# Optimization experiments

Hardware: AMD Instinct MI355X
Metric: run time of the kernel (lower is better)

Reference implementation:

```python
import jax, jax.numpy as jnp
import numpy as np

N_HEAD = 16
N_KV = 4
HEAD_DIM = 128
N_EMBD = 2048
GATE_CH = 32


def setup_inputs() -> dict:
    key = jax.random.key(0)
    ks = jax.random.split(key, 9)
    B, T = 2, 2048
    return {
        "x": jax.random.normal(ks[0], (B, T, N_EMBD), jnp.float32),
        "ve": jax.random.normal(ks[1], (B, T, N_KV * HEAD_DIM), jnp.float32),
        "cos": jax.random.uniform(ks[2], (T, 1, HEAD_DIM // 2), jnp.float32),
        "sin": jax.random.uniform(ks[3], (T, 1, HEAD_DIM // 2), jnp.float32),
        "wq": jax.random.normal(ks[4], (N_HEAD * HEAD_DIM, N_EMBD), jnp.float32) * 0.02,
        "wk": jax.random.normal(ks[5], (N_KV * HEAD_DIM, N_EMBD), jnp.float32) * 0.02,
        "wv": jax.random.normal(ks[6], (N_KV * HEAD_DIM, N_EMBD), jnp.float32) * 0.02,
        "wo": jax.random.normal(ks[7], (N_EMBD, N_EMBD), jnp.float32) * 0.02,
        "wgate": jax.random.normal(ks[8], (N_KV, GATE_CH), jnp.float32) * 0.02,
        "window_size": 512,
    }


def _rope(t, cos, sin):
    half = t.shape[-1] // 2
    t1, t2 = t[..., :half], t[..., half:]
    return jnp.concatenate([t1 * cos + t2 * sin, -t1 * sin + t2 * cos], axis=-1)


def _rms(t):
    eps = jnp.finfo(t.dtype).eps
    return t * jax.lax.rsqrt(jnp.mean(t * t, axis=-1, keepdims=True) + eps)


def reference(x, ve, cos, sin, wq, wk, wv, wo, wgate, window_size):
    B, T, _ = x.shape
    q = (x @ wq.T).reshape(B, T, N_HEAD, HEAD_DIM)
    k = (x @ wk.T).reshape(B, T, N_KV, HEAD_DIM)
    v = (x @ wv.T).reshape(B, T, N_KV, HEAD_DIM)
    # value-embedding gate
    gate = 2.0 * jax.nn.sigmoid(x[..., :GATE_CH] @ wgate.T)  # [B,T,N_KV]
    v = v + gate[..., None] * ve.reshape(B, T, N_KV, HEAD_DIM)
    # RoPE then QK RMSNorm
    q = _rms(_rope(q, cos, sin)).transpose(0, 2, 1, 3)  # [B,H,T,D]
    k = _rms(_rope(k, cos, sin)).transpose(0, 2, 1, 3)  # [B,KV,T,D]
    v = v.transpose(0, 2, 1, 3)
    rep = N_HEAD // N_KV
    k = jnp.repeat(k, rep, axis=1)  # repeat_interleave over head dim
    v = jnp.repeat(v, rep, axis=1)
    # sliding-window causal mask (past_len=0, key_len=T)
    pos = jnp.arange(T)
    mask = (pos[None, :] <= pos[:, None]) & (pos[None, :] >= pos[:, None] - window_size + 1)
    scale = 1.0 / jnp.sqrt(jnp.float32(HEAD_DIM))
    scores = jnp.einsum("bhqd,bhkd->bhqk", q, k) * scale
    scores = jnp.where(mask[None, None], scores, jnp.finfo(scores.dtype).min)
    attn = jax.nn.softmax(scores, axis=-1)
    y = jnp.einsum("bhqk,bhkd->bhqd", attn, v)
    y = y.transpose(0, 2, 1, 3).reshape(B, T, N_EMBD)
    return y @ wo.T
```

## Files before the change

### kernel.cpp

```cpp
#include <hip/hip_runtime.h>
#include <hip/hip_bf16.h>

typedef __attribute__((ext_vector_type(8))) short short8_t;
typedef __attribute__((ext_vector_type(4))) float f32x4;
typedef __attribute__((ext_vector_type(16))) float f32x16;
using bf16 = __hip_bfloat16;

#define MFMA_BF16(A, B, C) __builtin_amdgcn_mfma_f32_16x16x32_bf16((A), (B), (C), 0, 0, 0)
#define MFMA32_BF16(A, B, C) __builtin_amdgcn_mfma_f32_32x32x16_bf16((A), (B), (C), 0, 0, 0)

#define GLD_LDS16(g, l)                                                        \
  __builtin_amdgcn_global_load_lds(                                           \
      (const __attribute__((address_space(1))) unsigned int*)(const void*)(g),\
      (__attribute__((address_space(3))) unsigned int*)(void*)(l), 16, 0, 0)

__device__ __forceinline__ float bits2f(short s) {
  union { unsigned int u; float f; } c;
  c.u = ((unsigned int)(unsigned short)s) << 16;
  return c.f;
}
__device__ __forceinline__ short f2bits(float f) {
  bf16 h = __float2bfloat16(f);
  return *reinterpret_cast<short*>(&h);
}
__device__ __forceinline__ unsigned pack2(float lo, float hi) {
  return ((unsigned)(unsigned short)f2bits(lo)) |
         (((unsigned)(unsigned short)f2bits(hi)) << 16);
}
__device__ __forceinline__ float exp2_(float x) {
#if __has_builtin(__builtin_amdgcn_exp2f)
  return __builtin_amdgcn_exp2f(x);
#else
  return exp2f(x);
#endif
}

__global__ __launch_bounds__(256) void cvt_f32_bf16(const float* __restrict__ in,
                                                    short* __restrict__ out, int n) {
  int i = (blockIdx.x * 256 + threadIdx.x) * 4;
  if (i >= n) return;
  float4 v = *reinterpret_cast<const float4*>(in + i);
  short4 o;
  o.x = f2bits(v.x); o.y = f2bits(v.y); o.z = f2bits(v.z); o.w = f2bits(v.w);
  *reinterpret_cast<short4*>(out + i) = o;
}

__global__ __launch_bounds__(256) void cvt_w3(const float* __restrict__ wq,
                                              const float* __restrict__ wk,
                                              const float* __restrict__ wv,
                                              short* __restrict__ out) {
  int i = (blockIdx.x * 256 + threadIdx.x) * 4;
  const float* src;
  int off;
  if (i < 4194304) { src = wq; off = i; }
  else if (i < 5242880) { src = wk; off = i - 4194304; }
  else { src = wv; off = i - 5242880; }
  float4 v = *reinterpret_cast<const float4*>(src + off);
  short4 o;
  o.x = f2bits(v.x); o.y = f2bits(v.y); o.z = f2bits(v.z); o.w = f2bits(v.w);
  *reinterpret_cast<short4*>(out + i) = o;
}

template <int STORE_BF16>
__global__ __launch_bounds__(128, 2) void gemm_bt5(const short* __restrict__ A,
                                                   const short* __restrict__ Bt,
                                                   void* __restrict__ C,
                                                   int M, int N, int K, int NBN) {
  __shared__ __align__(16) short lds[3 * 8192];
  const int nwg = gridDim.x;
  const int cpx = nwg >> 3;
  const int wg = ((int)blockIdx.x & 7) * cpx + ((int)blockIdx.x >> 3);
  const int m0 = (wg / NBN) * 128, n0 = (wg % NBN) * 128;

  const int tid = threadIdx.x, w = tid >> 6, lane = tid & 63;
  const int rr = lane & 15, g = lane >> 4;

  const int srow = tid >> 2;
  const int sg = (tid & 3) ^ (srow & 3);
  const short* Asrc = A + (size_t)(m0 + srow) * K + sg * 8;
  const short* Bsrc = Bt + (size_t)(n0 + srow) * K + sg * 8;
  const int dofs = tid * 16;

  const int xorg = ((g ^ (rr & 3)) << 4);
  const int abase = rr * 64 + xorg;
  const int bbase = 8192 + w * 4096 + rr * 64 + xorg;

  f32x4 acc[8][4];
#pragma unroll
  for (int mi = 0; mi < 8; ++mi)
#pragma unroll
    for (int ni = 0; ni < 4; ++ni) acc[mi][ni] = (f32x4){0.f, 0.f, 0.f, 0.f};

  const int ns = K >> 5;

#define STG5(s_, base_) do {                                                   \
    const short* a_ = Asrc + (size_t)(s_) * 32;                                \
    const short* b_ = Bsrc + (size_t)(s_) * 32;                                \
    char* d_ = (char*)lds + (base_) + dofs;                                    \
    GLD_LDS16(a_,                  d_);                                        \
    GLD_LDS16(a_ + (size_t)32 * K, d_ + 2048);                                 \
    GLD_LDS16(a_ + (size_t)64 * K, d_ + 4096);                                 \
    GLD_LDS16(a_ + (size_t)96 * K, d_ + 6144);                                 \
    GLD_LDS16(b_,                  d_ + 8192);                                 \
    GLD_LDS16(b_ + (size_t)32 * K, d_ + 10240);                                \
    GLD_LDS16(b_ + (size_t)64 * K, d_ + 12288);                                \
    GLD_LDS16(b_ + (size_t)96 * K, d_ + 14336);                                \
  } while (0)

  STG5(0, 0);
  if (ns > 1) STG5(1, 16384);
  asm volatile("s_waitcnt vmcnt(8)" ::: "memory");
  asm volatile("s_barrier" ::: "memory");

  int c0 = 0, c1 = 16384, c2 = 32768;
  for (int s = 0; s < ns; ++s) {
    const char* bufp = (const char*)lds + c0;
    short8_t a0 = *(const short8_t*)(bufp + abase);
    short8_t a1 = *(const short8_t*)(bufp + abase + 1024);
    short8_t a2 = *(const short8_t*)(bufp + abase + 2048);
    short8_t a3 = *(const short8_t*)(bufp + abase + 3072);
    short8_t a4 = *(const short8_t*)(bufp + abase + 4096);
    short8_t a5 = *(const short8_t*)(bufp + abase + 5120);
    short8_t a6 = *(const short8_t*)(bufp + abase + 6144);
    short8_t a7 = *(const short8_t*)(bufp + abase + 7168);
    short8_t b0 = *(const short8_t*)(bufp + bbase);
    short8_t b1 = *(const short8_t*)(bufp + bbase + 1024);
    short8_t b2 = *(const short8_t*)(bufp + bbase + 2048);
    short8_t b3 = *(const short8_t*)(bufp + bbase + 3072);

    if (s + 2 < ns) STG5(s + 2, c2);

    asm volatile("s_waitcnt lgkmcnt(0)" ::: "memory");
    __builtin_amdgcn_sched_barrier(0);
    __builtin_amdgcn_s_setprio(1);
    acc[0][0] = MFMA_BF16(a0, b0, acc[0][0]);
    acc[0][1] = MFMA_BF16(a0, b1, acc[0][1]);
    acc[0][2] = MFMA_BF16(a0, b2, acc[0][2]);
    acc[0][3] = MFMA_BF16(a0, b3, acc[0][3]);
    acc[1][0] = MFMA_BF16(a1, b0, acc[1][0]);
    acc[1][1] = MFMA_BF16(a1, b1, acc[1][1]);
    acc[1][2] = MFMA_BF16(a1, b2, acc[1][2]);
    acc[1][3] = MFMA_BF16(a1, b3, acc[1][3]);
    acc[2][0] = MFMA_BF16(a2, b0, acc[2][0]);
    acc[2][1] = MFMA_BF16(a2, b1, acc[2][1]);
    acc[2][2] = MFMA_BF16(a2, b2, acc[2][2]);
    acc[2][3] = MFMA_BF16(a2, b3, acc[2][3]);
    acc[3][0] = MFMA_BF16(a3, b0, acc[3][0]);
    acc[3][1] = MFMA_BF16(a3, b1, acc[3][1]);
    acc[3][2] = MFMA_BF16(a3, b2, acc[3][2]);
    acc[3][3] = MFMA_BF16(a3, b3, acc[3][3]);
    acc[4][0] = MFMA_BF16(a4, b0, acc[4][0]);
    acc[4][1] = MFMA_BF16(a4, b1, acc[4][1]);
    acc[4][2] = MFMA_BF16(a4, b2, acc[4][2]);
    acc[4][3] = MFMA_BF16(a4, b3, acc[4][3]);
    acc[5][0] = MFMA_BF16(a5, b0, acc[5][0]);
    acc[5][1] = MFMA_BF16(a5, b1, acc[5][1]);
    acc[5][2] = MFMA_BF16(a5, b2, acc[5][2]);
    acc[5][3] = MFMA_BF16(a5, b3, acc[5][3]);
    acc[6][0] = MFMA_BF16(a6, b0, acc[6][0]);
    acc[6][1] = MFMA_BF16(a6, b1, acc[6][1]);
    acc[6][2] = MFMA_BF16(a6, b2, acc[6][2]);
    acc[6][3] = MFMA_BF16(a6, b3, acc[6][3]);
    acc[7][0] = MFMA_BF16(a7, b0, acc[7][0]);
    acc[7][1] = MFMA_BF16(a7, b1, acc[7][1]);
    acc[7][2] = MFMA_BF16(a7, b2, acc[7][2]);
    acc[7][3] = MFMA_BF16(a7, b3, acc[7][3]);
    __builtin_amdgcn_s_setprio(0);

    if (s + 2 < ns)
      asm volatile("s_waitcnt vmcnt(8)" ::: "memory");
    else if (s + 1 < ns)
      asm volatile("s_waitcnt vmcnt(0)" ::: "memory");
    asm volatile("s_barrier" ::: "memory");
    int t_ = c0; c0 = c1; c1 = c2; c2 = t_;
  }
#undef STG5

#pragma unroll
  for (int mi = 0; mi < 8; ++mi)
#pragma unroll
    for (int ni = 0; ni < 4; ++ni) {
      const int row = m0 + mi * 16 + g * 4;
      const int col = n0 + w * 64 + ni * 16 + rr;
#pragma unroll
      for (int j = 0; j < 4; ++j) {
        float v = acc[mi][ni][j];
        if (STORE_BF16)
          reinterpret_cast<short*>(C)[(size_t)(row + j) * N + col] = f2bits(v);
        else
          reinterpret_cast<float*>(C)[(size_t)(row + j) * N + col] = v;
      }
    }
}

__global__ __launch_bounds__(256) void rope_rms_qk(const short* __restrict__ qkv,
                                                   const float* __restrict__ cosT,
                                                   const float* __restrict__ sinT,
                                                   short* __restrict__ qO,
                                                   short* __restrict__ kO) {
  const int T = 2048;
  int unit = blockIdx.x * 4 + (threadIdx.x >> 6);
  int lane = threadIdx.x & 63;
  int hh = unit % 20;
  int t = (unit / 20) % T;
  int b = unit / (20 * T);
  int col = hh < 16 ? hh * 128 : 2048 + (hh - 16) * 128;
  const short* src = qkv + (size_t)(b * T + t) * 3072 + col;
  float t1 = bits2f(src[lane]), t2 = bits2f(src[lane + 64]);
  float c = cosT[t * 64 + lane], s = sinT[t * 64 + lane];
  float o1 = t1 * c + t2 * s;
  float o2 = t2 * c - t1 * s;
  float ss = o1 * o1 + o2 * o2;
#pragma unroll
  for (int o = 1; o < 64; o <<= 1) ss += __shfl_xor(ss, o, 64);
  float r = rsqrtf(ss * (1.f / 128.f) + 1.1920929e-07f);
  short* dst;
  if (hh < 16) {
    r *= 0.08838834764831845f * 1.4426950408889634f;
    dst = qO + ((size_t)(b * 16 + hh) * T + t) * 128;
  } else {
    dst = kO + ((size_t)(b * 4 + (hh - 16)) * T + t) * 128;
  }
  dst[lane] = f2bits(o1 * r);
  dst[lane + 64] = f2bits(o2 * r);
}

__global__ __launch_bounds__(256) void v_gate(const short* __restrict__ qkv,
                                              const float* __restrict__ x,
                                              const float* __restrict__ ve,
                                              const float* __restrict__ wgate,
                                              short* __restrict__ vO) {
  const int T = 2048;
  int unit = blockIdx.x * 4 + (threadIdx.x >> 6);
  int lane = threadIdx.x & 63;
  int kv = unit & 3;
  int t = (unit >> 2) % T;
  int b = unit / (4 * T);
  size_t m = (size_t)b * T + t;
  float z = 0.f;
  if (lane < 32) z = x[m * 2048 + lane] * wgate[kv * 32 + lane];
#pragma unroll
  for (int o = 1; o < 64; o <<= 1) z += __shfl_xor(z, o, 64);
  float gate = 2.f / (1.f + __expf(-z));
  const short* vsrc = qkv + m * 3072 + 2560 + kv * 128;
  const float* vesrc = ve + m * 512 + kv * 128;
  short* dst = vO + ((size_t)(b * 4 + kv) * T + t) * 128;
  dst[lane] = f2bits(bits2f(vsrc[lane]) + gate * vesrc[lane]);
  dst[lane + 64] = f2bits(bits2f(vsrc[lane + 64]) + gate * vesrc[lane + 64]);
}

__global__ __launch_bounds__(256) void v_transpose(const short* __restrict__ vp,
                                                   short* __restrict__ vT) {
  const int T = 2048;
  int bkv = blockIdx.x & 7;
  int t0 = (blockIdx.x >> 3) * 64;
  __shared__ __align__(16) short L[128 * 64];
  int tid = threadIdx.x;
  int tt = tid >> 2, dblk = tid & 3;
  const short* src = vp + ((size_t)bkv * T + t0 + tt) * 128 + dblk * 32;
  short8_t v0 = *(const short8_t*)(src);
  short8_t v1 = *(const short8_t*)(src + 8);
  short8_t v2 = *(const short8_t*)(src + 16);
  short8_t v3 = *(const short8_t*)(src + 24);
#pragma unroll
  for (int i = 0; i < 32; ++i) {
    int d = dblk * 32 + i;
    int byte = (d * 128 + tt * 2) ^ ((d & 7) << 4);
    short val = i < 8 ? v0[i] : i < 16 ? v1[i - 8] : i < 24 ? v2[i - 16] : v3[i - 24];
    *(short*)((char*)L + byte) = val;
  }
  __syncthreads();
  int d = tid >> 1, th = tid & 1;
  const char* Lp = (const char*)L;
#pragma unroll
  for (int g2 = 0; g2 < 4; ++g2) {
    short8_t o = *(const short8_t*)(Lp + ((d * 128 + th * 64 + g2 * 16) ^ ((d & 7) << 4)));
    *(short8_t*)(vT + ((size_t)bkv * 128 + d) * T + t0 + th * 32 + g2 * 8) = o;
  }
}

__global__ __launch_bounds__(256) void attn_sw3(const short* __restrict__ Q,
                                                const short* __restrict__ K,
                                                const short* __restrict__ VT,
                                                short* __restrict__ Y,
                                                const int* __restrict__ winp) {
  const int T = 2048, H = 16;
  const int win = *winp;
  int combo = blockIdx.x & 7;
  int j = blockIdx.x >> 3;
  int b = combo >> 2, kvh = combo & 3;
  int h = kvh * 4 + (j & 3);
  int q0 = (15 - (j >> 2)) * 128;

  __shared__ __align__(16) short Ks[2][64 * 128];
  __shared__ __align__(16) short Vs[2][128 * 64];

  int tid = threadIdx.x, w = tid >> 6, lane = tid & 63;
  int ql = lane & 31, hi = lane >> 5;
  int qrow = q0 + w * 32 + ql;

  const short* qbase = Q + ((size_t)(b * H + h) * T + qrow) * 128;
  short8_t qf[8];
#pragma unroll
  for (int ks = 0; ks < 8; ++ks)
    qf[ks] = *reinterpret_cast<const short8_t*>(qbase + ks * 16 + hi * 8);

  const short* kbase = K + (size_t)(b * 4 + kvh) * T * 128;
  const short* vtbase = VT + (size_t)(b * 4 + kvh) * 128 * T;

  f32x16 acc[4];
#pragma unroll
  for (int dt = 0; dt < 4; ++dt)
#pragma unroll
    for (int r = 0; r < 16; ++r) acc[dt][r] = 0.f;
  float mreg = -1e30f, lsum = 0.f;

  int lo = q0 - win + 1;
  if (lo < 0) lo = 0;
  lo &= ~63;
  const int nt = (q0 + 128 - lo) >> 6;
  int qmin = q0 + w * 32, qmax = qmin + 31;

#define STAGE_A(ti, bi) do {                                                   \
    int kc_ = lo + (ti) * 64;                                                  \
    _Pragma("unroll")                                                          \
    for (int r = 0; r < 4; ++r) {                                              \
      int slot = (r * 4 + w) * 64 + lane;                                      \
      int krow = slot >> 4;                                                    \
      int gc = (slot & 15) ^ (krow & 7);                                       \
      GLD_LDS16(kbase + (size_t)(kc_ + krow) * 128 + gc * 8,                   \
                (char*)Ks[bi] + (r * 4 + w) * 1024);                           \
    }                                                                          \
    _Pragma("unroll")                                                          \
    for (int r = 0; r < 4; ++r) {                                              \
      int slot = (r * 4 + w) * 64 + lane;                                      \
      int d_ = slot >> 3;                                                      \
      int gc = (slot & 7) ^ (d_ & 7);                                          \
      GLD_LDS16(vtbase + (size_t)d_ * T + kc_ + gc * 8,                        \
                (char*)Vs[bi] + (r * 4 + w) * 1024);                           \
    }                                                                          \
  } while (0)

  STAGE_A(0, 0);

  int cur = 0;
  for (int t = 0; t < nt; ++t) {
    if (t + 1 < nt) {
      STAGE_A(t + 1, cur ^ 1);
      asm volatile("s_waitcnt vmcnt(8)" ::: "memory");
    } else {
      asm volatile("s_waitcnt vmcnt(0)" ::: "memory");
    }
    asm volatile("s_barrier" ::: "memory");

    int kc = lo + t * 64;
    bool active = (kc <= qmax) && (kc + 63 >= qmin - win + 1);
    if (active) {
      const char* Kp = (const char*)Ks[cur];
      const char* Vp = (const char*)Vs[cur];
      f32x16 sA[2];
#pragma unroll
      for (int r = 0; r < 16; ++r) { sA[0][r] = 0.f; sA[1][r] = 0.f; }
#pragma unroll
      for (int kt = 0; kt < 2; ++kt) {
        int kr = kt * 32 + ql;
#pragma unroll
        for (int ks = 0; ks < 8; ++ks) {
          int byte = kr * 256 + (((ks * 2 + hi) ^ (kr & 7)) << 4);
          short8_t kf = *reinterpret_cast<const short8_t*>(Kp + byte);
          sA[kt] = MFMA32_BF16(kf, qf[ks], sA[kt]);
        }
      }
      float pmax = -1e30f;
#pragma unroll
      for (int kt = 0; kt < 2; ++kt)
#pragma unroll
        for (int r = 0; r < 16; ++r) {
          int key = kc + kt * 32 + (r & 3) + 8 * (r >> 2) + 4 * hi;
          float sv = sA[kt][r];
          sv = ((unsigned)(qrow - key) < (unsigned)win) ? sv : -1e30f;
          sA[kt][r] = sv;
          pmax = fmaxf(pmax, sv);
        }
      pmax = fmaxf(pmax, __shfl_xor(pmax, 32, 64));
      float mn = fmaxf(mreg, pmax);
      float corr = exp2_(mreg - mn);
      mreg = mn;
      float rs = 0.f;
#pragma unroll
      for (int kt = 0; kt < 2; ++kt)
#pragma unroll
        for (int r = 0; r < 16; ++r) {
          float p = exp2_(sA[kt][r] - mn);
          sA[kt][r] = p;
          rs += p;
        }
      rs += __shfl_xor(rs, 32, 64);
      lsum = lsum * corr + rs;
#pragma unroll
      for (int dt = 0; dt < 4; ++dt)
#pragma unroll
        for (int r = 0; r < 16; ++r) acc[dt][r] *= corr;

#pragma unroll
      for (int kt = 0; kt < 2; ++kt)
#pragma unroll
        for (int s = 0; s < 2; ++s) {
          unsigned a = pack2(sA[kt][8 * s + 0], sA[kt][8 * s + 1]);
          unsigned bb = pack2(sA[kt][8 * s + 2], sA[kt][8 * s + 3]);
          unsigned c = pack2(sA[kt][8 * s + 4], sA[kt][8 * s + 5]);
          unsigned dd = pack2(sA[kt][8 * s + 6], sA[kt][8 * s + 7]);
          unsigned sa = __shfl_xor(a, 32, 64);
          unsigned sb = __shfl_xor(bb, 32, 64);
          unsigned sc2 = __shfl_xor(c, 32, 64);
          unsigned sd = __shfl_xor(dd, 32, 64);
          union { unsigned u[4]; short8_t s8; } pu;
          pu.u[0] = hi ? sc2 : a;
          pu.u[1] = hi ? sd : bb;
          pu.u[2] = hi ? c : sa;
          pu.u[3] = hi ? dd : sb;
          const int kst = kt * 2 + s;
#pragma unroll
          for (int dt = 0; dt < 4; ++dt) {
            int d_ = dt * 32 + ql;
            int byte = (d_ << 7) + ((((kst * 2 + hi)) ^ (d_ & 7)) << 4);
            short8_t vf = *reinterpret_cast<const short8_t*>(Vp + byte);
            acc[dt] = MFMA32_BF16(vf, pu.s8, acc[dt]);
          }
        }
    }
    asm volatile("s_barrier" ::: "memory");
    cur ^= 1;
  }
#undef STAGE_A

  float rinv = 1.f / lsum;
  short* ybase = Y + ((size_t)(b * T + qrow) * H + h) * 128;
#pragma unroll
  for (int dt = 0; dt < 4; ++dt)
#pragma unroll
    for (int g2 = 0; g2 < 4; ++g2) {
      short4 o;
      o.x = f2bits(acc[dt][g2 * 4 + 0] * rinv);
      o.y = f2bits(acc[dt][g2 * 4 + 1] * rinv);
      o.z = f2bits(acc[dt][g2 * 4 + 2] * rinv);
      o.w = f2bits(acc[dt][g2 * 4 + 3] * rinv);
      *reinterpret_cast<short4*>(ybase + dt * 32 + 8 * g2 + 4 * hi) = o;
    }
}

extern "C" void kernel_launch(void* const* d_in, const int* in_sizes, int n_in,
                              void* d_out, int out_size, void* d_ws, size_t ws_size,
                              hipStream_t stream) {
  const float* x = (const float*)d_in[0];
  const float* ve = (const float*)d_in[1];
  const float* cosT = (const float*)d_in[2];
  const float* sinT = (const float*)d_in[3];
  const float* wq = (const float*)d_in[4];
  const float* wk = (const float*)d_in[5];
  const float* wv = (const float*)d_in[6];
  const float* wo = (const float*)d_in[7];
  const float* wgate = (const float*)d_in[8];
  const int* winp = (const int*)d_in[9];
  float* out = (float*)d_out;
  char* ws = (char*)d_ws;

  const int B = 2, T = 2048;
  short* xb    = (short*)(ws);
  short* wqkvb = (short*)(ws + 16777216);
  short* wob   = (short*)(ws + 29360128);
  short* qkv   = (short*)(ws + 37748736);
  short* qpost = (short*)(ws + 62914560);
  short* kpost = (short*)(ws + 79691776);
  short* vpost = (short*)(ws + 83886080);
  short* ybuf  = (short*)(ws + 88080384);
  short* vTb   = qkv;

  cvt_f32_bf16<<<dim3(8192), 256, 0, stream>>>(x, xb, B * T * 2048);
  cvt_w3<<<dim3(6144), 256, 0, stream>>>(wq, wk, wv, wqkvb);
  cvt_f32_bf16<<<dim3(4096), 256, 0, stream>>>(wo, wob, 2048 * 2048);

  gemm_bt5<1><<<dim3(768), 128, 0, stream>>>(xb, wqkvb, qkv, 4096, 3072, 2048, 24);

  rope_rms_qk<<<dim3(B * T * 20 / 4), 256, 0, stream>>>(qkv, cosT, sinT, qpost, kpost);
  v_gate<<<dim3(B * T), 256, 0, stream>>>(qkv, x, ve, wgate, vpost);
  v_transpose<<<dim3(8 * (T / 64)), 256, 0, stream>>>(vpost, vTb);

  attn_sw3<<<dim3(512), 256, 0, stream>>>(qpost, kpost, vTb, ybuf, winp);

  gemm_bt5<0><<<dim3(512), 128, 0, stream>>>(ybuf, wob, out, 4096, 2048, 2048, 16);
}
```

Before: 197.3 us.

## Enlarge GEMM tile to 256x128 with 4 waves and fuse V gate with transpose

The GEMM now uses 256-thread workgroups computing 256x128 tiles, with a 2x2 wave layout. The three-stage LDS ring is restructured so the next stage's global-to-LDS loads are issued in two halves interleaved with two MFMA phases, and there is a single barrier per iteration. Separately, the value-embedding gate and the V transpose are fused into one kernel, which removes an intermediate buffer round-trip and a launch. Larger tiles halve the grid (384 and 256 blocks), which risks worse CU occupancy and tail balance on a 256-CU part.

```diff
diff --git a/kernel.cpp b/kernel.cpp
--- a/kernel.cpp
+++ b/kernel.cpp
@@ -62,28 +62,29 @@
 }
 
 template <int STORE_BF16>
-__global__ __launch_bounds__(128, 2) void gemm_bt5(const short* __restrict__ A,
+__global__ __launch_bounds__(256, 2) void gemm_bt6(const short* __restrict__ A,
                                                    const short* __restrict__ Bt,
                                                    void* __restrict__ C,
                                                    int M, int N, int K, int NBN) {
-  __shared__ __align__(16) short lds[3 * 8192];
+  __shared__ __align__(16) short lds[3 * 12288];
   const int nwg = gridDim.x;
   const int cpx = nwg >> 3;
   const int wg = ((int)blockIdx.x & 7) * cpx + ((int)blockIdx.x >> 3);
-  const int m0 = (wg / NBN) * 128, n0 = (wg % NBN) * 128;
+  const int m0 = (wg / NBN) * 256, n0 = (wg % NBN) * 128;
 
   const int tid = threadIdx.x, w = tid >> 6, lane = tid & 63;
+  const int wm = w >> 1, wn = w & 1;
   const int rr = lane & 15, g = lane >> 4;
 
-  const int srow = tid >> 2;
-  const int sg = (tid & 3) ^ (srow & 3);
-  const short* Asrc = A + (size_t)(m0 + srow) * K + sg * 8;
-  const short* Bsrc = Bt + (size_t)(n0 + srow) * K + sg * 8;
+  const int srow4 = tid >> 2;
+  const int scol = ((tid & 3) ^ (srow4 & 3)) * 8;
+  const short* Asrc = A + (size_t)(m0 + srow4) * K + scol;
+  const short* Bsrc = Bt + (size_t)(n0 + srow4) * K + scol;
+  const size_t rstep = (size_t)64 * K;
   const int dofs = tid * 16;
 
-  const int xorg = ((g ^ (rr & 3)) << 4);
-  const int abase = rr * 64 + xorg;
-  const int bbase = 8192 + w * 4096 + rr * 64 + xorg;
+  const int abase = ((((wm * 128 + rr) << 6) | (g << 4)) ^ ((rr & 3) << 4));
+  const int bbase = 16384 + ((((wn * 64 + rr) << 6) | (g << 4)) ^ ((rr & 3) << 4));
 
   f32x4 acc[8][4];
 #pragma unroll
@@ -93,95 +94,110 @@
 
   const int ns = K >> 5;
 
-#define STG5(s_, base_) do {                                                   \
+#define STG_FULL(s_, base_) do {                                               \
     const short* a_ = Asrc + (size_t)(s_) * 32;                                \
     const short* b_ = Bsrc + (size_t)(s_) * 32;                                \
     char* d_ = (char*)lds + (base_) + dofs;                                    \
-    GLD_LDS16(a_,                  d_);                                        \
-    GLD_LDS16(a_ + (size_t)32 * K, d_ + 2048);                                 \
-    GLD_LDS16(a_ + (size_t)64 * K, d_ + 4096);                                 \
-    GLD_LDS16(a_ + (size_t)96 * K, d_ + 6144);                                 \
-    GLD_LDS16(b_,                  d_ + 8192);                                 \
-    GLD_LDS16(b_ + (size_t)32 * K, d_ + 10240);                                \
-    GLD_LDS16(b_ + (size_t)64 * K, d_ + 12288);                                \
-    GLD_LDS16(b_ + (size_t)96 * K, d_ + 14336);                                \
+    GLD_LDS16(a_,             d_);                                             \
+    GLD_LDS16(a_ + rstep,     d_ + 4096);                                      \
+    GLD_LDS16(a_ + 2 * rstep, d_ + 8192);                                      \
+    GLD_LDS16(a_ + 3 * rstep, d_ + 12288);                                     \
+    GLD_LDS16(b_,             d_ + 16384);                                     \
+    GLD_LDS16(b_ + rstep,     d_ + 20480);                                     \
   } while (0)
 
-  STG5(0, 0);
-  if (ns > 1) STG5(1, 16384);
-  asm volatile("s_waitcnt vmcnt(8)" ::: "memory");
-  asm volatile("s_barrier" ::: "memory");
-
-  int c0 = 0, c1 = 16384, c2 = 32768;
+  STG_FULL(0, 0);
+  if (ns > 1) STG_FULL(1, 24576);
+  asm volatile("s_waitcnt vmcnt(6)" ::: "memory");
+
+  int sl = 0;
   for (int s = 0; s < ns; ++s) {
-    const char* bufp = (const char*)lds + c0;
-    short8_t a0 = *(const short8_t*)(bufp + abase);
-    short8_t a1 = *(const short8_t*)(bufp + abase + 1024);
-    short8_t a2 = *(const short8_t*)(bufp + abase + 2048);
-    short8_t a3 = *(const short8_t*)(bufp + abase + 3072);
-    short8_t a4 = *(const short8_t*)(bufp + abase + 4096);
-    short8_t a5 = *(const short8_t*)(bufp + abase + 5120);
-    short8_t a6 = *(const short8_t*)(bufp + abase + 6144);
-    short8_t a7 = *(const short8_t*)(bufp + abase + 7168);
-    short8_t b0 = *(const short8_t*)(bufp + bbase);
-    short8_t b1 = *(const short8_t*)(bufp + bbase + 1024);
-    short8_t b2 = *(const short8_t*)(bufp + bbase + 2048);
-    short8_t b3 = *(const short8_t*)(bufp + bbase + 3072);
-
-    if (s + 2 < ns) STG5(s + 2, c2);
-
+    asm volatile("s_barrier" ::: "memory");
+    const char* Ap = (const char*)lds + sl;
+    int sl2 = sl + 49152; if (sl2 >= 73728) sl2 -= 73728;
+    const bool more = (s + 2) < ns;
+    const short* a2 = Asrc + (size_t)(s + 2) * 32;
+    const short* b2 = Bsrc + (size_t)(s + 2) * 32;
+    char* d2 = (char*)lds + sl2 + dofs;
+
+    short8_t b0 = *(const short8_t*)(Ap + bbase);
+    short8_t b1 = *(const short8_t*)(Ap + bbase + 1024);
+    short8_t b2f = *(const short8_t*)(Ap + bbase + 2048);
+    short8_t b3 = *(const short8_t*)(Ap + bbase + 3072);
+    short8_t a0 = *(const short8_t*)(Ap + abase);
+    short8_t a1 = *(const short8_t*)(Ap + abase + 1024);
+    short8_t a2f = *(const short8_t*)(Ap + abase + 2048);
+    short8_t a3 = *(const short8_t*)(Ap + abase + 3072);
+    if (more) {
+      GLD_LDS16(a2, d2);
+      GLD_LDS16(a2 + rstep, d2 + 4096);
+    }
     asm volatile("s_waitcnt lgkmcnt(0)" ::: "memory");
     __builtin_amdgcn_sched_barrier(0);
     __builtin_amdgcn_s_setprio(1);
     acc[0][0] = MFMA_BF16(a0, b0, acc[0][0]);
     acc[0][1] = MFMA_BF16(a0, b1, acc[0][1]);
-    acc[0][2] = MFMA_BF16(a0, b2, acc[0][2]);
+    acc[0][2] = MFMA_BF16(a0, b2f, acc[0][2]);
     acc[0][3] = MFMA_BF16(a0, b3, acc[0][3]);
     acc[1][0] = MFMA_BF16(a1, b0, acc[1][0]);
     acc[1][1] = MFMA_BF16(a1, b1, acc[1][1]);
-    acc[1][2] = MFMA_BF16(a1, b2, acc[1][2]);
+    acc[1][2] = MFMA_BF16(a1, b2f, acc[1][2]);
     acc[1][3] = MFMA_BF16(a1, b3, acc[1][3]);
-    acc[2][0] = MFMA_BF16(a2, b0, acc[2][0]);
-    acc[2][1] = MFMA_BF16(a2, b1, acc[2][1]);
-    acc[2][2] = MFMA_BF16(a2, b2, acc[2][2]);
-    acc[2][3] = MFMA_BF16(a2, b3, acc[2][3]);
+    acc[2][0] = MFMA_BF16(a2f, b0, acc[2][0]);
+    acc[2][1] = MFMA_BF16(a2f, b1, acc[2][1]);
+    acc[2][2] = MFMA_BF16(a2f, b2f, acc[2][2]);
+    acc[2][3] = MFMA_BF16(a2f, b3, acc[2][3]);
     acc[3][0] = MFMA_BF16(a3, b0, acc[3][0]);
     acc[3][1] = MFMA_BF16(a3, b1, acc[3][1]);
-    acc[3][2] = MFMA_BF16(a3, b2, acc[3][2]);
+    acc[3][2] = MFMA_BF16(a3, b2f, acc[3][2]);
     acc[3][3] = MFMA_BF16(a3, b3, acc[3][3]);
+    __builtin_amdgcn_s_setprio(0);
+
+    short8_t a4 = *(const short8_t*)(Ap + abase + 4096);
+    short8_t a5 = *(const short8_t*)(Ap + abase + 5120);
+    short8_t a6 = *(const short8_t*)(Ap + abase + 6144);
+    short8_t a7 = *(const short8_t*)(Ap + abase + 7168);
+    if (more) {
+      GLD_LDS16(a2 + 2 * rstep, d2 + 8192);
+      GLD_LDS16(a2 + 3 * rstep, d2 + 12288);
+      GLD_LDS16(b2, d2 + 16384);
+      GLD_LDS16(b2 + rstep, d2 + 20480);
+    }
+    asm volatile("s_waitcnt lgkmcnt(0)" ::: "memory");
+    __builtin_amdgcn_sched_barrier(0);
+    __builtin_amdgcn_s_setprio(1);
     acc[4][0] = MFMA_BF16(a4, b0, acc[4][0]);
     acc[4][1] = MFMA_BF16(a4, b1, acc[4][1]);
-    acc[4][2] = MFMA_BF16(a4, b2, acc[4][2]);
+    acc[4][2] = MFMA_BF16(a4, b2f, acc[4][2]);
     acc[4][3] = MFMA_BF16(a4, b3, acc[4][3]);
     acc[5][0] = MFMA_BF16(a5, b0, acc[5][0]);
     acc[5][1] = MFMA_BF16(a5, b1, acc[5][1]);
-    acc[5][2] = MFMA_BF16(a5, b2, acc[5][2]);
+    acc[5][2] = MFMA_BF16(a5, b2f, acc[5][2]);
     acc[5][3] = MFMA_BF16(a5, b3, acc[5][3]);
     acc[6][0] = MFMA_BF16(a6, b0, acc[6][0]);
     acc[6][1] = MFMA_BF16(a6, b1, acc[6][1]);
-    acc[6][2] = MFMA_BF16(a6, b2, acc[6][2]);
+    acc[6][2] = MFMA_BF16(a6, b2f, acc[6][2]);
     acc[6][3] = MFMA_BF16(a6, b3, acc[6][3]);
     acc[7][0] = MFMA_BF16(a7, b0, acc[7][0]);
     acc[7][1] = MFMA_BF16(a7, b1, acc[7][1]);
-    acc[7][2] = MFMA_BF16(a7, b2, acc[7][2]);
+    acc[7][2] = MFMA_BF16(a7, b2f, acc[7][2]);
     acc[7][3] = MFMA_BF16(a7, b3, acc[7][3]);
     __builtin_amdgcn_s_setprio(0);
 
-    if (s + 2 < ns)
-      asm volatile("s_waitcnt vmcnt(8)" ::: "memory");
+    if (more)
+      asm volatile("s_waitcnt vmcnt(6)" ::: "memory");
     else if (s + 1 < ns)
       asm volatile("s_waitcnt vmcnt(0)" ::: "memory");
-    asm volatile("s_barrier" ::: "memory");
-    int t_ = c0; c0 = c1; c1 = c2; c2 = t_;
+    sl += 24576; if (sl >= 73728) sl -= 73728;
   }
-#undef STG5
+#undef STG_FULL
 
 #pragma unroll
   for (int mi = 0; mi < 8; ++mi)
 #pragma unroll
     for (int ni = 0; ni < 4; ++ni) {
-      const int row = m0 + mi * 16 + g * 4;
-      const int col = n0 + w * 64 + ni * 16 + rr;
+      const int row = m0 + wm * 128 + mi * 16 + g * 4;
+      const int col = n0 + wn * 64 + ni * 16 + rr;
 #pragma unroll
       for (int j = 0; j < 4; ++j) {
         float v = acc[mi][ni][j];
@@ -225,49 +241,43 @@
   dst[lane + 64] = f2bits(o2 * r);
 }
 
-__global__ __launch_bounds__(256) void v_gate(const short* __restrict__ qkv,
-                                              const float* __restrict__ x,
-                                              const float* __restrict__ ve,
-                                              const float* __restrict__ wgate,
-                                              short* __restrict__ vO) {
-  const int T = 2048;
-  int unit = blockIdx.x * 4 + (threadIdx.x >> 6);
-  int lane = threadIdx.x & 63;
-  int kv = unit & 3;
-  int t = (unit >> 2) % T;
-  int b = unit / (4 * T);
-  size_t m = (size_t)b * T + t;
-  float z = 0.f;
-  if (lane < 32) z = x[m * 2048 + lane] * wgate[kv * 32 + lane];
-#pragma unroll
-  for (int o = 1; o < 64; o <<= 1) z += __shfl_xor(z, o, 64);
-  float gate = 2.f / (1.f + __expf(-z));
-  const short* vsrc = qkv + m * 3072 + 2560 + kv * 128;
-  const float* vesrc = ve + m * 512 + kv * 128;
-  short* dst = vO + ((size_t)(b * 4 + kv) * T + t) * 128;
-  dst[lane] = f2bits(bits2f(vsrc[lane]) + gate * vesrc[lane]);
-  dst[lane + 64] = f2bits(bits2f(vsrc[lane + 64]) + gate * vesrc[lane + 64]);
-}
-
-__global__ __launch_bounds__(256) void v_transpose(const short* __restrict__ vp,
-                                                   short* __restrict__ vT) {
+__global__ __launch_bounds__(256) void vgate_t(const short* __restrict__ qkv,
+                                               const float* __restrict__ x,
+                                               const float* __restrict__ ve,
+                                               const float* __restrict__ wgate,
+                                               short* __restrict__ vT) {
   const int T = 2048;
   int bkv = blockIdx.x & 7;
   int t0 = (blockIdx.x >> 3) * 64;
+  int b = bkv >> 2, kv = bkv & 3;
   __shared__ __align__(16) short L[128 * 64];
   int tid = threadIdx.x;
-  int tt = tid >> 2, dblk = tid & 3;
-  const short* src = vp + ((size_t)bkv * T + t0 + tt) * 128 + dblk * 32;
-  short8_t v0 = *(const short8_t*)(src);
-  short8_t v1 = *(const short8_t*)(src + 8);
-  short8_t v2 = *(const short8_t*)(src + 16);
-  short8_t v3 = *(const short8_t*)(src + 24);
+  int tt = tid >> 2, q = tid & 3;
+  size_t m = (size_t)b * T + t0 + tt;
+  float z = 0.f;
+  const float* xp = x + m * 2048 + q * 8;
+  const float* wgp = wgate + kv * 32 + q * 8;
+#pragma unroll
+  for (int i = 0; i < 8; ++i) z += xp[i] * wgp[i];
+  z += __shfl_xor(z, 1, 64);
+  z += __shfl_xor(z, 2, 64);
+  float gate = 2.f / (1.f + __expf(-z));
+  const short* vsrc = qkv + m * 3072 + 2560 + kv * 128 + q * 32;
+  const float* vesrc = ve + m * 512 + kv * 128 + q * 32;
+  short8_t v0 = *(const short8_t*)(vsrc);
+  short8_t v1 = *(const short8_t*)(vsrc + 8);
+  short8_t v2 = *(const short8_t*)(vsrc + 16);
+  short8_t v3 = *(const short8_t*)(vsrc + 24);
+  float4 e[8];
+#pragma unroll
+  for (int i = 0; i < 8; ++i) e[i] = *(const float4*)(vesrc + i * 4);
 #pragma unroll
   for (int i = 0; i < 32; ++i) {
-    int d = dblk * 32 + i;
+    int d = q * 32 + i;
+    short vv = i < 8 ? v0[i] : i < 16 ? v1[i - 8] : i < 24 ? v2[i - 16] : v3[i - 24];
+    float ev = (&e[i >> 2].x)[i & 3];
     int byte = (d * 128 + tt * 2) ^ ((d & 7) << 4);
-    short val = i < 8 ? v0[i] : i < 16 ? v1[i - 8] : i < 24 ? v2[i - 16] : v3[i - 24];
-    *(short*)((char*)L + byte) = val;
+    *(short*)((char*)L + byte) = f2bits(bits2f(vv) + gate * ev);
   }
   __syncthreads();
   int d = tid >> 1, th = tid & 1;
@@ -472,21 +482,19 @@
   short* qkv   = (short*)(ws + 37748736);
   short* qpost = (short*)(ws + 62914560);
   short* kpost = (short*)(ws + 79691776);
-  short* vpost = (short*)(ws + 83886080);
+  short* vTb   = (short*)(ws + 83886080);
   short* ybuf  = (short*)(ws + 88080384);
-  short* vTb   = qkv;
 
   cvt_f32_bf16<<<dim3(8192), 256, 0, stream>>>(x, xb, B * T * 2048);
   cvt_w3<<<dim3(6144), 256, 0, stream>>>(wq, wk, wv, wqkvb);
   cvt_f32_bf16<<<dim3(4096), 256, 0, stream>>>(wo, wob, 2048 * 2048);
 
-  gemm_bt5<1><<<dim3(768), 128, 0, stream>>>(xb, wqkvb, qkv, 4096, 3072, 2048, 24);
+  gemm_bt6<1><<<dim3(384), 256, 0, stream>>>(xb, wqkvb, qkv, 4096, 3072, 2048, 24);
 
   rope_rms_qk<<<dim3(B * T * 20 / 4), 256, 0, stream>>>(qkv, cosT, sinT, qpost, kpost);
-  v_gate<<<dim3(B * T), 256, 0, stream>>>(qkv, x, ve, wgate, vpost);
-  v_transpose<<<dim3(8 * (T / 64)), 256, 0, stream>>>(vpost, vTb);
+  vgate_t<<<dim3(8 * (T / 64)), 256, 0, stream>>>(qkv, x, ve, wgate, vTb);
 
   attn_sw3<<<dim3(512), 256, 0, stream>>>(qpost, kpost, vTb, ybuf, winp);
 
-  gemm_bt5<0><<<dim3(512), 128, 0, stream>>>(ybuf, wob, out, 4096, 2048, 2048, 16);
-}
+  gemm_bt6<0><<<dim3(256), 256, 0, stream>>>(ybuf, wob, out, 4096, 2048, 2048, 16);
+}
```

Measured after the change: 187.9 us. 1.05x faster.
